# Kernel optimization log

Hardware: AMD Instinct MI355X
Metric: run time of the kernel (lower is better)

## Reference

```python
import jax, jax.numpy as jnp
import numpy as np

# Fixed problem sizes (equal-sized batch segments, matching setup_inputs)
B, N, M = 4, 4096, 16384          # clouds, coarse pts/cloud, fine pts/cloud
C_IN, C_SKIP, K = 256, 256, 3     # feature dims, knn k
CH = [C_IN + C_SKIP, 512, 256]    # MLP channels
EPS = 1e-16


def setup_inputs() -> dict:
    key = jax.random.key(0)
    ks = jax.random.split(key, 6)
    x = jax.random.normal(ks[0], (B * N, C_IN), jnp.float32)
    pos = jax.random.uniform(ks[1], (B * N, 3), jnp.float32)
    batch = jnp.repeat(jnp.arange(B, dtype=jnp.int64), N)
    x_skip = jax.random.normal(ks[2], (B * M, C_SKIP), jnp.float32)
    pos_skip = jax.random.uniform(ks[3], (B * M, 3), jnp.float32)
    batch_skip = jnp.repeat(jnp.arange(B, dtype=jnp.int64), M)
    W1 = jax.random.normal(ks[4], (CH[0], CH[1]), jnp.float32) / np.sqrt(CH[0]).astype(np.float32)
    b1 = jnp.zeros((CH[1],), jnp.float32)
    W2 = jax.random.normal(ks[5], (CH[1], CH[2]), jnp.float32) / np.sqrt(CH[1]).astype(np.float32)
    b2 = jnp.zeros((CH[2],), jnp.float32)
    return dict(x=x, pos=pos, batch=batch, x_skip=x_skip, pos_skip=pos_skip,
                batch_skip=batch_skip, W1=W1, b1=b1, W2=W2, b2=b2)


def _knn_interpolate(x, pos, pos_skip):
    """torch_geometric.nn.knn_interpolate with equal-sized batch segments."""
    xb = x.reshape(B, N, C_IN)
    ps = pos.reshape(B, N, 3)
    qs = pos_skip.reshape(B, M, 3)
    # squared pairwise distances [B, M, N]
    d2 = (jnp.sum(qs * qs, -1)[:, :, None]
          - 2.0 * jnp.einsum('bmd,bnd->bmn', qs, ps)
          + jnp.sum(ps * ps, -1)[:, None, :])
    neg_d2, idx = jax.lax.top_k(-d2, K)                # k smallest distances, [B,M,K]
    w = 1.0 / jnp.clip(-neg_d2, EPS)                   # inverse squared distance weights
    feats = jax.vmap(lambda f, i: f[i])(xb, idx)       # gather: [B, M, K, C_IN]
    y = jnp.sum(w[..., None] * feats, axis=2) / jnp.sum(w, axis=2)[..., None]
    return y.reshape(B * M, C_IN)


def reference(x, pos, batch, x_skip, pos_skip, batch_skip, W1, b1, W2, b2):
    y = _knn_interpolate(x, pos, pos_skip)
    h = jnp.concatenate([y, x_skip], axis=1)           # [B*M, 512]
    h = jax.nn.relu(h @ W1 + b1)
    h = jax.nn.relu(h @ W2 + b2)
    return h, pos_skip, batch_skip
```

## Files before the change

kernel.cpp:

```cpp
#include <hip/hip_runtime.h>
#include <stdint.h>

#define NB 4
#define NPTS 4096
#define MPTS 16384
#define CIN 256
#define CH0 512
#define CH1 512
#define CH2 256
#define ROWS (NB * MPTS)
#define POS_OUT_OFF (ROWS * CH2)
#define BATCH_OUT_OFF (POS_OUT_OFF + ROWS * 3)
#define CELL_CAP 40
#define QCAP 96

using u16 = unsigned short;
using u32 = unsigned int;
using u64 = unsigned long long;

typedef __bf16 bf16x8 __attribute__((ext_vector_type(8)));
typedef float f32x4 __attribute__((ext_vector_type(4)));

__device__ __forceinline__ u16 f2bf(float f) {
  u32 u = __builtin_bit_cast(u32, f);
  u32 r = u + 0x7fffu + ((u >> 16) & 1u);
  return (u16)(r >> 16);
}

__device__ __forceinline__ u32 flipf(float f) {
  u32 u = __builtin_bit_cast(u32, f);
  return u ^ ((u32)((int)u >> 31) | 0x80000000u);
}
__device__ __forceinline__ float unflipf(u32 f) {
  u32 m = (~(u32)((int)f >> 31)) | 0x80000000u;
  return __builtin_bit_cast(float, f ^ m);
}

__device__ __forceinline__ void ins3(u64 v, u64& k0, u64& k1, u64& k2) {
  u64 a = k0 < v ? v : k0;
  k0 = k0 < v ? k0 : v;
  u64 bb = k1 < a ? a : k1;
  k1 = k1 < a ? k1 : a;
  k2 = k2 < bb ? k2 : bb;
}

__device__ __forceinline__ void merge3(u64 r0, u64 r1, u64 r2,
                                       u64& k0, u64& k1, u64& k2) {
  u64 t = k0 < r0 ? r0 : k0;
  k0 = k0 < r0 ? k0 : r0;
  u64 u = k1 < r1 ? k1 : r1;
  u64 mtu = t < u ? u : t;
  k1 = t < u ? t : u;
  u64 v = k2 < r2 ? k2 : r2;
  k2 = mtu < v ? mtu : v;
}

__device__ __forceinline__ u64 shfl_xor_u64_w8(u64 v, int mask) {
  u32 lo = (u32)v, hi = (u32)(v >> 32);
  lo = (u32)__shfl_xor((int)lo, mask, 8);
  hi = (u32)__shfl_xor((int)hi, mask, 8);
  return ((u64)hi << 32) | lo;
}

__global__ __launch_bounds__(256) void preptail_kernel(
    const float* __restrict__ W1, const float* __restrict__ W2,
    u16* __restrict__ W1s, u16* __restrict__ W2s,
    const float* __restrict__ pos_skip, const int* __restrict__ batch_skip,
    float* __restrict__ out) {
  const int bid = blockIdx.x;
  if (bid < 192) {
    const int t = bid * 256 + threadIdx.x;
    if (t < 32768) {
      const int l = t & 63, ni = (t >> 6) & 3, wd = (t >> 8) & 7, kt = t >> 11;
      const int fr = l & 15, g = l >> 4;
      const int n = wd * 64 + ni * 16 + fr;
      u16 o[8];
#pragma unroll
      for (int j = 0; j < 8; ++j)
        o[j] = f2bf(W1[(kt * 32 + g * 8 + j) * CH1 + n]);
      *(uint4*)(W1s + (size_t)t * 8) = *(const uint4*)o;
    } else {
      const int c = t - 32768;
      const int l = c & 63, ni = (c >> 6) & 1, wd = (c >> 7) & 7, kt = c >> 10;
      const int fr = l & 15, g = l >> 4;
      const int n = wd * 32 + ni * 16 + fr;
      u16 o[8];
#pragma unroll
      for (int j = 0; j < 8; ++j)
        o[j] = f2bf(W2[(kt * 32 + g * 8 + j) * CH2 + n]);
      *(uint4*)(W2s + (size_t)c * 8) = *(const uint4*)o;
    }
  } else {
    const int t = (bid - 192) * 256 + threadIdx.x;
    if (t < ROWS * 3) {
      out[POS_OUT_OFF + t] = pos_skip[t];
    } else {
      int u = t - ROWS * 3;
      out[BATCH_OUT_OFF + u] = (float)batch_skip[u];
    }
  }
}

__global__ __launch_bounds__(256) void bin_kernel(
    const float* __restrict__ pos, float4* __restrict__ pts4,
    u32* __restrict__ cellCnt, int* __restrict__ cellIdx,
    const float* __restrict__ pos_skip, u32* __restrict__ qCnt,
    int* __restrict__ qIdx) {
#pragma clang fp contract(off)
  if (blockIdx.x < 64) {
    const int i = blockIdx.x * 256 + threadIdx.x;
    const float x = pos[i * 3 + 0], y = pos[i * 3 + 1], z = pos[i * 3 + 2];
    pts4[i] = make_float4(x, y, z, (x * x + y * y) + z * z);
    const int b = i >> 12;
    int cx = (int)(x * 8.0f); cx = cx < 0 ? 0 : (cx > 7 ? 7 : cx);
    int cy = (int)(y * 8.0f); cy = cy < 0 ? 0 : (cy > 7 ? 7 : cy);
    int cz = (int)(z * 8.0f); cz = cz < 0 ? 0 : (cz > 7 ? 7 : cz);
    const int c = b * 512 + cz * 64 + cy * 8 + cx;
    const u32 slot = atomicAdd(&cellCnt[c], 1u);
    if (slot < CELL_CAP) cellIdx[c * CELL_CAP + slot] = i;
  } else {
    const int q = (blockIdx.x - 64) * 256 + threadIdx.x;
    const int b = q >> 14;
    const float qx = pos_skip[q * 3 + 0];
    const float qy = pos_skip[q * 3 + 1];
    const float qz = pos_skip[q * 3 + 2];
    int cx = (int)(qx * 8.0f); cx = cx < 0 ? 0 : (cx > 7 ? 7 : cx);
    int cy = (int)(qy * 8.0f); cy = cy < 0 ? 0 : (cy > 7 ? 7 : cy);
    int cz = (int)(qz * 8.0f); cz = cz < 0 ? 0 : (cz > 7 ? 7 : cz);
    const int c = b * 512 + cz * 64 + cy * 8 + cx;
    const u32 slot = atomicAdd(&qCnt[c], 1u);
    if (slot < QCAP) qIdx[c * QCAP + slot] = q;
  }
}

__global__ __launch_bounds__(256) void knn_kernel(
    const float4* __restrict__ pts4, const u32* __restrict__ cellCnt,
    const int* __restrict__ cellIdx, const u32* __restrict__ qCnt,
    const int* __restrict__ qIdx, const float* __restrict__ pos_skip,
    int* __restrict__ idx_out, float* __restrict__ w_out,
    int* __restrict__ qPerm) {
#pragma clang fp contract(off)
  __shared__ float4 scand[27 * CELL_CAP];
  __shared__ int    scgi[27 * CELL_CAP];
  __shared__ u32    scnt[27];
  __shared__ int    sbase[27];
  __shared__ u32    nCand;
  __shared__ u32    ssc[256];
  const int tid = threadIdx.x;

  if (blockIdx.x >= 2048) {
    const int b = blockIdx.x - 2048;
    u32 c0 = qCnt[b * 512 + 2 * tid];     c0 = c0 > QCAP ? QCAP : c0;
    u32 c1 = qCnt[b * 512 + 2 * tid + 1]; c1 = c1 > QCAP ? QCAP : c1;
    const u32 ps = c0 + c1;
    u32 run = ps;
    ssc[tid] = run;
    for (int off = 1; off < 256; off <<= 1) {
      __syncthreads();
      u32 t = (tid >= off) ? ssc[tid - off] : 0u;
      __syncthreads();
      run += t;
      ssc[tid] = run;
    }
    const u32 excl = run - ps;
    const int base = b * MPTS + (int)excl;
    const int s0 = (b * 512 + 2 * tid) * QCAP;
    const int s1 = (b * 512 + 2 * tid + 1) * QCAP;
    for (u32 j = 0; j < c0; ++j) qPerm[base + j] = qIdx[s0 + j];
    for (u32 j = 0; j < c1; ++j) qPerm[base + c0 + j] = qIdx[s1 + j];
    return;
  }

  const int b = blockIdx.x >> 9;
  const int cell = blockIdx.x & 511;
  const int cz = cell >> 6, cy = (cell >> 3) & 7, cx = cell & 7;
  const int x0 = cx > 0 ? cx - 1 : 0, x1 = cx < 7 ? cx + 1 : 7;
  const int y0 = cy > 0 ? cy - 1 : 0, y1 = cy < 7 ? cy + 1 : 7;
  const int z0 = cz > 0 ? cz - 1 : 0, z1 = cz < 7 ? cz + 1 : 7;
  const int nx = x1 - x0 + 1, ny = y1 - y0 + 1, nz = z1 - z0 + 1;
  const int ncells = nx * ny * nz;
  if (tid == 0) nCand = 0;
  if (tid < ncells) {
    const int lz = tid / (nx * ny);
    const int rem = tid - lz * nx * ny;
    const int ly = rem / nx;
    const int lx = rem - ly * nx;
    const int cg = b * 512 + (z0 + lz) * 64 + (y0 + ly) * 8 + (x0 + lx);
    u32 cnt = cellCnt[cg];
    scnt[tid] = cnt > CELL_CAP ? CELL_CAP : cnt;
    sbase[tid] = cg * CELL_CAP;
  }
  __syncthreads();
  const int slots = ncells * CELL_CAP;
  for (int s = tid; s < slots; s += 256) {
    const int ci = s / CELL_CAP;
    const int sl = s - ci * CELL_CAP;
    if ((u32)sl < scnt[ci]) {
      const int gi = cellIdx[sbase[ci] + sl];
      const float4 p = pts4[gi];
      const u32 d = atomicAdd(&nCand, 1u);
      scand[d] = p;
      scgi[d] = gi;
    }
  }
  __syncthreads();
  const int nC = (int)nCand;
  u32 nq = qCnt[b * 512 + cell];
  if (nq > QCAP) nq = QCAP;
  const int qbase = (b * 512 + cell) * QCAP;
  const int g = tid >> 3;
  const int sub = tid & 7;

  for (int r0q = 0; r0q < (int)nq; r0q += 32) {
    const int qslot = r0q + g;
    if (qslot < (int)nq) {
      const int q = qIdx[qbase + qslot];
      const float qx = pos_skip[q * 3 + 0];
      const float qy = pos_skip[q * 3 + 1];
      const float qz = pos_skip[q * 3 + 2];
      const float q2 = (qx * qx + qy * qy) + qz * qz;
      u64 k0 = ~0ull, k1 = ~0ull, k2 = ~0ull;
      for (int s = sub; s < nC; s += 8) {
        const float4 p = scand[s];
        const float dot = fmaf(qz, p.z, fmaf(qy, p.y, qx * p.x));
        const float tv = (q2 - 2.0f * dot) + p.w;
        const u64 key = ((u64)flipf(tv) << 32) | (u32)scgi[s];
        ins3(key, k0, k1, k2);
      }
#pragma unroll
      for (int mask = 1; mask < 8; mask <<= 1) {
        const u64 r0 = shfl_xor_u64_w8(k0, mask);
        const u64 r1 = shfl_xor_u64_w8(k1, mask);
        const u64 r2 = shfl_xor_u64_w8(k2, mask);
        merge3(r0, r1, r2, k0, k1, k2);
      }
      float m2tv = unflipf((u32)(k2 >> 32));
      if (!(m2tv <= 0.015625f - 1e-5f)) {
        k0 = k1 = k2 = ~0ull;
        const int ex0 = cx > 1 ? cx - 2 : 0, ex1 = cx < 6 ? cx + 2 : 7;
        const int ey0 = cy > 1 ? cy - 2 : 0, ey1 = cy < 6 ? cy + 2 : 7;
        const int ez0 = cz > 1 ? cz - 2 : 0, ez1 = cz < 6 ? cz + 2 : 7;
        for (int zz = ez0; zz <= ez1; ++zz)
          for (int yy = ey0; yy <= ey1; ++yy)
            for (int xx = ex0; xx <= ex1; ++xx) {
              const int cg = b * 512 + zz * 64 + yy * 8 + xx;
              u32 cnt = cellCnt[cg];
              if (cnt > CELL_CAP) cnt = CELL_CAP;
              const int cb = cg * CELL_CAP;
              for (int s = sub; s < (int)cnt; s += 8) {
                const int gi = cellIdx[cb + s];
                const float4 p = pts4[gi];
                const float dot = fmaf(qz, p.z, fmaf(qy, p.y, qx * p.x));
                const float tv = (q2 - 2.0f * dot) + p.w;
                ins3(((u64)flipf(tv) << 32) | (u32)gi, k0, k1, k2);
              }
            }
#pragma unroll
        for (int mask = 1; mask < 8; mask <<= 1) {
          const u64 r0 = shfl_xor_u64_w8(k0, mask);
          const u64 r1 = shfl_xor_u64_w8(k1, mask);
          const u64 r2 = shfl_xor_u64_w8(k2, mask);
          merge3(r0, r1, r2, k0, k1, k2);
        }
        m2tv = unflipf((u32)(k2 >> 32));
        if (!(m2tv <= 0.0625f - 1e-5f)) {
          k0 = k1 = k2 = ~0ull;
          const int base = b * NPTS;
          for (int i = sub; i < NPTS; i += 8) {
            const int gi = base + i;
            const float4 p = pts4[gi];
            const float dot = fmaf(qz, p.z, fmaf(qy, p.y, qx * p.x));
            const float tv = (q2 - 2.0f * dot) + p.w;
            ins3(((u64)flipf(tv) << 32) | (u32)gi, k0, k1, k2);
          }
#pragma unroll
          for (int mask = 1; mask < 8; mask <<= 1) {
            const u64 r0 = shfl_xor_u64_w8(k0, mask);
            const u64 r1 = shfl_xor_u64_w8(k1, mask);
            const u64 r2 = shfl_xor_u64_w8(k2, mask);
            merge3(r0, r1, r2, k0, k1, k2);
          }
        }
      }
      if (sub == 0) {
        const float t0 = unflipf((u32)(k0 >> 32));
        const float t1 = unflipf((u32)(k1 >> 32));
        const float t2 = unflipf((u32)(k2 >> 32));
        const float w0 = 1.0f / fmaxf(t0, 1e-16f);
        const float w1 = 1.0f / fmaxf(t1, 1e-16f);
        const float w2 = 1.0f / fmaxf(t2, 1e-16f);
        const float wsum = (w0 + w1) + w2;
        const float inv = 1.0f / wsum;
        idx_out[q * 3 + 0] = (int)(u32)k0;
        idx_out[q * 3 + 1] = (int)(u32)k1;
        idx_out[q * 3 + 2] = (int)(u32)k2;
        w_out[q * 3 + 0] = w0 * inv;
        w_out[q * 3 + 1] = w1 * inv;
        w_out[q * 3 + 2] = w2 * inv;
      }
    }
  }
}

__global__ __launch_bounds__(512, 2) void fused_mlp_kernel(
    const float* __restrict__ x, const int* __restrict__ idx,
    const float* __restrict__ w, const float* __restrict__ x_skip,
    const u16* __restrict__ W1s, const float* __restrict__ b1,
    const u16* __restrict__ W2s, const float* __restrict__ b2,
    const int* __restrict__ qPerm, float* __restrict__ out) {
  __shared__ __align__(16) u16 Abuf[128 * 512];
  __shared__ int sPerm[128];
  const int tid = threadIdx.x;
  const int m0 = blockIdx.x * 128;

  if (tid < 128) sPerm[tid] = qPerm[m0 + tid];

#pragma unroll
  for (int p = 0; p < 2; ++p) {
    const int row = p * 64 + (tid >> 3);
    const int sub = tid & 7;
    const int gr = qPerm[m0 + row];
    u16* rowp = Abuf + row * 512;
    const int rx = row & 7;
    if (sub < 4) {
      const int i0 = idx[gr * 3 + 0], i1 = idx[gr * 3 + 1], i2 = idx[gr * 3 + 2];
      const float w0 = w[gr * 3 + 0], w1 = w[gr * 3 + 1], w2 = w[gr * 3 + 2];
      const float4* p0 = (const float4*)(x + (size_t)i0 * CIN + sub * 64);
      const float4* p1 = (const float4*)(x + (size_t)i1 * CIN + sub * 64);
      const float4* p2 = (const float4*)(x + (size_t)i2 * CIN + sub * 64);
#pragma unroll
      for (int c = 0; c < 8; ++c) {
        const float4 a0 = p0[c * 2], a1 = p1[c * 2], a2 = p2[c * 2];
        const float4 d0 = p0[c * 2 + 1], d1 = p1[c * 2 + 1], d2 = p2[c * 2 + 1];
        u16 o[8];
        o[0] = f2bf(fmaf(w0, a0.x, fmaf(w1, a1.x, w2 * a2.x)));
        o[1] = f2bf(fmaf(w0, a0.y, fmaf(w1, a1.y, w2 * a2.y)));
        o[2] = f2bf(fmaf(w0, a0.z, fmaf(w1, a1.z, w2 * a2.z)));
        o[3] = f2bf(fmaf(w0, a0.w, fmaf(w1, a1.w, w2 * a2.w)));
        o[4] = f2bf(fmaf(w0, d0.x, fmaf(w1, d1.x, w2 * d2.x)));
        o[5] = f2bf(fmaf(w0, d0.y, fmaf(w1, d1.y, w2 * d2.y)));
        o[6] = f2bf(fmaf(w0, d0.z, fmaf(w1, d1.z, w2 * d2.z)));
        o[7] = f2bf(fmaf(w0, d0.w, fmaf(w1, d1.w, w2 * d2.w)));
        const int pp = ((c & 3) << 3) | (((2 * sub + (c >> 2)) ^ rx) & 7);
        *(uint4*)(rowp + pp * 8) = *(const uint4*)o;
      }
    } else {
      const int ss = sub - 4;
      const float4* ps = (const float4*)(x_skip + (size_t)gr * CIN + ss * 64);
#pragma unroll
      for (int c = 0; c < 8; ++c) {
        const float4 a = ps[c * 2], d = ps[c * 2 + 1];
        u16 o[8];
        o[0] = f2bf(a.x); o[1] = f2bf(a.y); o[2] = f2bf(a.z); o[3] = f2bf(a.w);
        o[4] = f2bf(d.x); o[5] = f2bf(d.y); o[6] = f2bf(d.z); o[7] = f2bf(d.w);
        const int pp = 32 | ((c & 3) << 3) | (((2 * ss + (c >> 2)) ^ rx) & 7);
        *(uint4*)(rowp + pp * 8) = *(const uint4*)o;
      }
    }
  }
  __syncthreads();

  const int wid = tid >> 6;
  const int lane = tid & 63;
  const int fr = lane & 15;
  const int g = lane >> 4;
  const int frx = fr & 7;

  f32x4 acc[8][4];
#pragma unroll
  for (int mi = 0; mi < 8; mi++)
#pragma unroll
    for (int ni = 0; ni < 4; ni++) acc[mi][ni] = (f32x4){0.f, 0.f, 0.f, 0.f};

  {
    const u16* B1 = W1s + wid * 2048 + lane * 8;
    bf16x8 bf[2][4];
#pragma unroll
    for (int ni = 0; ni < 4; ni++)
      bf[0][ni] = *(const bf16x8*)(B1 + ni * 512);
    for (int kt = 0; kt < 16; ++kt) {
      const int cur = kt & 1;
      if (kt < 15) {
        const u16* nb = B1 + (kt + 1) * 16384;
#pragma unroll
        for (int ni = 0; ni < 4; ni++)
          bf[cur ^ 1][ni] = *(const bf16x8*)(nb + ni * 512);
      }
#pragma unroll
      for (int mi = 0; mi < 8; mi++) {
        const bf16x8 af = *(const bf16x8*)&Abuf[(mi * 16 + fr) * 512 +
            ((((kt >> 3) << 5) | (g << 3) | ((kt & 7) ^ frx)) * 8)];
#pragma unroll
        for (int ni = 0; ni < 4; ni++)
          acc[mi][ni] = __builtin_amdgcn_mfma_f32_16x16x32_bf16(
              af, bf[cur][ni], acc[mi][ni], 0, 0, 0);
      }
    }
  }
  __syncthreads();

  {
    const int wn = wid * 64;
#pragma unroll
    for (int ni = 0; ni < 4; ni++) {
      const int n = wn + ni * 16 + fr;
      const float bb = b1[n];
      const int vg = n >> 3;
      const int nlow = n & 7;
      const int pb = (vg & 32) | ((vg & 3) << 3) | ((vg >> 2) & 7);
#pragma unroll
      for (int mi = 0; mi < 8; mi++) {
#pragma unroll
        for (int r = 0; r < 4; r++) {
          const int m = mi * 16 + g * 4 + r;
          const float v = fmaxf(acc[mi][ni][r] + bb, 0.f);
          Abuf[m * 512 + (pb ^ (m & 7)) * 8 + nlow] = f2bf(v);
        }
      }
    }
  }
  __syncthreads();

  f32x4 acc2[8][2];
#pragma unroll
  for (int mi = 0; mi < 8; mi++)
#pragma unroll
    for (int ni = 0; ni < 2; ni++) acc2[mi][ni] = (f32x4){0.f, 0.f, 0.f, 0.f};

  {
    const u16* B2 = W2s + wid * 1024 + lane * 8;
    bf16x8 bf[2][2];
#pragma unroll
    for (int ni = 0; ni < 2; ni++)
      bf[0][ni] = *(const bf16x8*)(B2 + ni * 512);
    for (int kt = 0; kt < 16; ++kt) {
      const int cur = kt & 1;
      if (kt < 15) {
        const u16* nb = B2 + (kt + 1) * 8192;
#pragma unroll
        for (int ni = 0; ni < 2; ni++)
          bf[cur ^ 1][ni] = *(const bf16x8*)(nb + ni * 512);
      }
#pragma unroll
      for (int mi = 0; mi < 8; mi++) {
        const bf16x8 af = *(const bf16x8*)&Abuf[(mi * 16 + fr) * 512 +
            ((((kt >> 3) << 5) | (g << 3) | ((kt & 7) ^ frx)) * 8)];
#pragma unroll
        for (int ni = 0; ni < 2; ni++)
          acc2[mi][ni] = __builtin_amdgcn_mfma_f32_16x16x32_bf16(
              af, bf[cur][ni], acc2[mi][ni], 0, 0, 0);
      }
    }
  }

#pragma unroll
  for (int ni = 0; ni < 2; ni++) {
    const int col = wid * 32 + ni * 16 + fr;
    const float bb = b2[col];
#pragma unroll
    for (int mi = 0; mi < 8; mi++) {
#pragma unroll
      for (int r = 0; r < 4; r++) {
        const int rowg = sPerm[mi * 16 + g * 4 + r];
        out[(size_t)rowg * CH2 + col] = fmaxf(acc2[mi][ni][r] + bb, 0.f);
      }
    }
  }
}

extern "C" void kernel_launch(void* const* d_in, const int* in_sizes, int n_in,
                              void* d_out, int out_size, void* d_ws, size_t ws_size,
                              hipStream_t stream) {
  const float* x        = (const float*)d_in[0];
  const float* pos      = (const float*)d_in[1];
  const float* x_skip   = (const float*)d_in[3];
  const float* pos_skip = (const float*)d_in[4];
  const int*   batch_sk = (const int*)d_in[5];
  const float* W1       = (const float*)d_in[6];
  const float* b1       = (const float*)d_in[7];
  const float* W2       = (const float*)d_in[8];
  const float* b2       = (const float*)d_in[9];
  float* out = (float*)d_out;

  char* ws = (char*)d_ws;
  u16*    W1s     = (u16*)(ws);
  u16*    W2s     = (u16*)(ws + 524288);
  int*    idxb    = (int*)(ws + 786432);
  float*  wb      = (float*)(ws + 1572864);
  float4* pts4    = (float4*)(ws + 2359296);
  u32*    cellCnt = (u32*)(ws + 2621440);
  u32*    qCnt    = (u32*)(ws + 2629632);
  int*    cellIdx = (int*)(ws + 2637824);
  int*    qIdx    = (int*)(ws + 2965504);
  int*    qPerm   = (int*)(ws + 3751936);

  hipMemsetAsync(cellCnt, 0, 16384, stream);
  preptail_kernel<<<dim3(1216), dim3(256), 0, stream>>>(
      W1, W2, W1s, W2s, pos_skip, batch_sk, out);
  bin_kernel<<<dim3(320), dim3(256), 0, stream>>>(
      pos, pts4, cellCnt, cellIdx, pos_skip, qCnt, qIdx);
  knn_kernel<<<dim3(2052), dim3(256), 0, stream>>>(pts4, cellCnt, cellIdx,
                                                   qCnt, qIdx, pos_skip,
                                                   idxb, wb, qPerm);
  fused_mlp_kernel<<<dim3(512), dim3(512), 0, stream>>>(
      x, idxb, wb, x_skip, W1s, b1, W2s, b2, qPerm, out);
}
```

Before: 263.7 us.

## Deduplicate kNN neighbor gathers via shared-memory hash and halve MLP row tile

The fused MLP kernel now processes 64 rows per block instead of 128, launching twice as many blocks. For each 32-row half it builds a small shared-memory hash table of unique neighbor indices, loads each unique coarse feature row once as bf16 into LDS, then interpolates from LDS. It also prefetches all A fragments before the MFMA loop. The aim is to cut redundant global gathers for spatially sorted queries and to improve occupancy and load balance. The cost is more barriers and atomics, halved weight reuse per block, and interpolating from bf16-rounded inputs, which adds a little extra rounding.

```diff
diff --git a/kernel.cpp b/kernel.cpp
--- a/kernel.cpp
+++ b/kernel.cpp
@@ -25,6 +25,10 @@
   u32 u = __builtin_bit_cast(u32, f);
   u32 r = u + 0x7fffu + ((u >> 16) & 1u);
   return (u16)(r >> 16);
+}
+
+__device__ __forceinline__ float bf2f(u16 h) {
+  return __builtin_bit_cast(float, (u32)h << 16);
 }
 
 __device__ __forceinline__ u32 flipf(float f) {
@@ -302,63 +306,111 @@
   }
 }
 
-__global__ __launch_bounds__(512, 2) void fused_mlp_kernel(
+__global__ __launch_bounds__(512) void fused_mlp_kernel(
     const float* __restrict__ x, const int* __restrict__ idx,
     const float* __restrict__ w, const float* __restrict__ x_skip,
     const u16* __restrict__ W1s, const float* __restrict__ b1,
     const u16* __restrict__ W2s, const float* __restrict__ b2,
     const int* __restrict__ qPerm, float* __restrict__ out) {
-  __shared__ __align__(16) u16 Abuf[128 * 512];
-  __shared__ int sPerm[128];
+  __shared__ __align__(16) u16 Abuf[64 * 512];
+  __shared__ __align__(16) u16 Xs[96 * 264];
+  __shared__ int   sPerm[64];
+  __shared__ float sWt[96];
+  __shared__ int   sSlot[96];
+  __shared__ int   hKey[128];
+  __shared__ int   hVal[128];
+  __shared__ int   uList[96];
+  __shared__ u32   uCnt;
   const int tid = threadIdx.x;
-  const int m0 = blockIdx.x * 128;
-
-  if (tid < 128) sPerm[tid] = qPerm[m0 + tid];
-
-#pragma unroll
+  const int m0 = blockIdx.x * 64;
+
+  if (tid < 64) sPerm[tid] = qPerm[m0 + tid];
+
   for (int p = 0; p < 2; ++p) {
-    const int row = p * 64 + (tid >> 3);
-    const int sub = tid & 7;
-    const int gr = qPerm[m0 + row];
-    u16* rowp = Abuf + row * 512;
-    const int rx = row & 7;
-    if (sub < 4) {
-      const int i0 = idx[gr * 3 + 0], i1 = idx[gr * 3 + 1], i2 = idx[gr * 3 + 2];
-      const float w0 = w[gr * 3 + 0], w1 = w[gr * 3 + 1], w2 = w[gr * 3 + 2];
-      const float4* p0 = (const float4*)(x + (size_t)i0 * CIN + sub * 64);
-      const float4* p1 = (const float4*)(x + (size_t)i1 * CIN + sub * 64);
-      const float4* p2 = (const float4*)(x + (size_t)i2 * CIN + sub * 64);
-#pragma unroll
-      for (int c = 0; c < 8; ++c) {
-        const float4 a0 = p0[c * 2], a1 = p1[c * 2], a2 = p2[c * 2];
-        const float4 d0 = p0[c * 2 + 1], d1 = p1[c * 2 + 1], d2 = p2[c * 2 + 1];
+    if (tid < 128) hKey[tid] = -1;
+    if (tid == 0) uCnt = 0;
+    __syncthreads();
+    int myH = 0;
+    if (tid < 96) {
+      const int r = tid / 3, k = tid - r * 3;
+      const int q = sPerm[p * 32 + r];
+      const int key = idx[q * 3 + k];
+      sWt[tid] = w[q * 3 + k];
+      u32 h = (((u32)key * 2654435761u) >> 25) & 127u;
+      for (;;) {
+        const int prev = atomicCAS(&hKey[h], -1, key);
+        if (prev == -1) {
+          const int s = (int)atomicAdd(&uCnt, 1u);
+          hVal[h] = s;
+          uList[s] = key;
+          myH = (int)h;
+          break;
+        }
+        if (prev == key) { myH = (int)h; break; }
+        h = (h + 1) & 127u;
+      }
+    }
+    __syncthreads();
+    const int U = (int)uCnt;
+    if (tid < 96) sSlot[tid] = hVal[myH];
+    if (tid < 256) {
+      for (int j = tid; j < U * 64; j += 256) {
+        const int u = j >> 6, seg = j & 63;
+        const float4 v = ((const float4*)x)[(size_t)uList[u] * 64 + seg];
+        u16 o[4] = {f2bf(v.x), f2bf(v.y), f2bf(v.z), f2bf(v.w)};
+        *(uint2*)&Xs[u * 264 + seg * 4] = *(const uint2*)o;
+      }
+    } else {
+      const int t2 = tid - 256;
+      for (int j = t2; j < 32 * 64; j += 256) {
+        const int r = j >> 6, seg = j & 63;
+        const int row = p * 32 + r;
+        const float4 v = ((const float4*)x_skip)[(size_t)sPerm[row] * 64 + seg];
+        u16 o[4] = {f2bf(v.x), f2bf(v.y), f2bf(v.z), f2bf(v.w)};
+        const int s5 = seg >> 1;
+        const int c = s5 & 3, ss = s5 >> 2;
+        const int pp = 32 | (c << 3) | ((ss ^ (row & 7)) & 7);
+        *(uint2*)&Abuf[row * 512 + pp * 8 + (seg & 1) * 4] = *(const uint2*)o;
+      }
+    }
+    __syncthreads();
+    if (tid < 256) {
+      const int r = tid >> 3, sub = tid & 7;
+      const int row = p * 32 + r;
+      const int e = r * 3;
+      const int s0 = sSlot[e], s1 = sSlot[e + 1], s2 = sSlot[e + 2];
+      const float w0 = sWt[e], w1 = sWt[e + 1], w2 = sWt[e + 2];
+      const u16* x0 = &Xs[s0 * 264 + sub * 32];
+      const u16* x1 = &Xs[s1 * 264 + sub * 32];
+      const u16* x2 = &Xs[s2 * 264 + sub * 32];
+      const int rx = row & 7;
+      u16* rowp = Abuf + row * 512;
+#pragma unroll
+      for (int c = 0; c < 4; ++c) {
+        const uint4 v0 = *(const uint4*)(x0 + c * 8);
+        const uint4 v1 = *(const uint4*)(x1 + c * 8);
+        const uint4 v2 = *(const uint4*)(x2 + c * 8);
+        const u32 a0[4] = {v0.x, v0.y, v0.z, v0.w};
+        const u32 a1[4] = {v1.x, v1.y, v1.z, v1.w};
+        const u32 a2[4] = {v2.x, v2.y, v2.z, v2.w};
         u16 o[8];
-        o[0] = f2bf(fmaf(w0, a0.x, fmaf(w1, a1.x, w2 * a2.x)));
-        o[1] = f2bf(fmaf(w0, a0.y, fmaf(w1, a1.y, w2 * a2.y)));
-        o[2] = f2bf(fmaf(w0, a0.z, fmaf(w1, a1.z, w2 * a2.z)));
-        o[3] = f2bf(fmaf(w0, a0.w, fmaf(w1, a1.w, w2 * a2.w)));
-        o[4] = f2bf(fmaf(w0, d0.x, fmaf(w1, d1.x, w2 * d2.x)));
-        o[5] = f2bf(fmaf(w0, d0.y, fmaf(w1, d1.y, w2 * d2.y)));
-        o[6] = f2bf(fmaf(w0, d0.z, fmaf(w1, d1.z, w2 * d2.z)));
-        o[7] = f2bf(fmaf(w0, d0.w, fmaf(w1, d1.w, w2 * d2.w)));
-        const int pp = ((c & 3) << 3) | (((2 * sub + (c >> 2)) ^ rx) & 7);
+#pragma unroll
+        for (int jj = 0; jj < 4; ++jj) {
+          const float lo = fmaf(w0, __builtin_bit_cast(float, a0[jj] << 16),
+                          fmaf(w1, __builtin_bit_cast(float, a1[jj] << 16),
+                          w2 * __builtin_bit_cast(float, a2[jj] << 16)));
+          const float hi = fmaf(w0, __builtin_bit_cast(float, a0[jj] & 0xffff0000u),
+                          fmaf(w1, __builtin_bit_cast(float, a1[jj] & 0xffff0000u),
+                          w2 * __builtin_bit_cast(float, a2[jj] & 0xffff0000u)));
+          o[jj * 2]     = f2bf(lo);
+          o[jj * 2 + 1] = f2bf(hi);
+        }
+        const int pp = (c << 3) | ((sub ^ rx) & 7);
         *(uint4*)(rowp + pp * 8) = *(const uint4*)o;
       }
-    } else {
-      const int ss = sub - 4;
-      const float4* ps = (const float4*)(x_skip + (size_t)gr * CIN + ss * 64);
-#pragma unroll
-      for (int c = 0; c < 8; ++c) {
-        const float4 a = ps[c * 2], d = ps[c * 2 + 1];
-        u16 o[8];
-        o[0] = f2bf(a.x); o[1] = f2bf(a.y); o[2] = f2bf(a.z); o[3] = f2bf(a.w);
-        o[4] = f2bf(d.x); o[5] = f2bf(d.y); o[6] = f2bf(d.z); o[7] = f2bf(d.w);
-        const int pp = 32 | ((c & 3) << 3) | (((2 * ss + (c >> 2)) ^ rx) & 7);
-        *(uint4*)(rowp + pp * 8) = *(const uint4*)o;
-      }
-    }
-  }
-  __syncthreads();
+    }
+    __syncthreads();
+  }
 
   const int wid = tid >> 6;
   const int lane = tid & 63;
@@ -366,9 +418,9 @@
   const int g = lane >> 4;
   const int frx = fr & 7;
 
-  f32x4 acc[8][4];
-#pragma unroll
-  for (int mi = 0; mi < 8; mi++)
+  f32x4 acc[4][4];
+#pragma unroll
+  for (int mi = 0; mi < 4; mi++)
 #pragma unroll
     for (int ni = 0; ni < 4; ni++) acc[mi][ni] = (f32x4){0.f, 0.f, 0.f, 0.f};
 
@@ -386,15 +438,17 @@
         for (int ni = 0; ni < 4; ni++)
           bf[cur ^ 1][ni] = *(const bf16x8*)(nb + ni * 512);
       }
-#pragma unroll
-      for (int mi = 0; mi < 8; mi++) {
-        const bf16x8 af = *(const bf16x8*)&Abuf[(mi * 16 + fr) * 512 +
+      bf16x8 af[4];
+#pragma unroll
+      for (int mi = 0; mi < 4; mi++)
+        af[mi] = *(const bf16x8*)&Abuf[(mi * 16 + fr) * 512 +
             ((((kt >> 3) << 5) | (g << 3) | ((kt & 7) ^ frx)) * 8)];
+#pragma unroll
+      for (int mi = 0; mi < 4; mi++)
 #pragma unroll
         for (int ni = 0; ni < 4; ni++)
           acc[mi][ni] = __builtin_amdgcn_mfma_f32_16x16x32_bf16(
-              af, bf[cur][ni], acc[mi][ni], 0, 0, 0);
-      }
+              af[mi], bf[cur][ni], acc[mi][ni], 0, 0, 0);
     }
   }
   __syncthreads();
@@ -409,7 +463,7 @@
       const int nlow = n & 7;
       const int pb = (vg & 32) | ((vg & 3) << 3) | ((vg >> 2) & 7);
 #pragma unroll
-      for (int mi = 0; mi < 8; mi++) {
+      for (int mi = 0; mi < 4; mi++) {
 #pragma unroll
         for (int r = 0; r < 4; r++) {
           const int m = mi * 16 + g * 4 + r;
@@ -421,9 +475,9 @@
   }
   __syncthreads();
 
-  f32x4 acc2[8][2];
-#pragma unroll
-  for (int mi = 0; mi < 8; mi++)
+  f32x4 acc2[4][2];
+#pragma unroll
+  for (int mi = 0; mi < 4; mi++)
 #pragma unroll
     for (int ni = 0; ni < 2; ni++) acc2[mi][ni] = (f32x4){0.f, 0.f, 0.f, 0.f};
 
@@ -441,15 +495,17 @@
         for (int ni = 0; ni < 2; ni++)
           bf[cur ^ 1][ni] = *(const bf16x8*)(nb + ni * 512);
       }
-#pragma unroll
-      for (int mi = 0; mi < 8; mi++) {
-        const bf16x8 af = *(const bf16x8*)&Abuf[(mi * 16 + fr) * 512 +
+      bf16x8 af[4];
+#pragma unroll
+      for (int mi = 0; mi < 4; mi++)
+        af[mi] = *(const bf16x8*)&Abuf[(mi * 16 + fr) * 512 +
             ((((kt >> 3) << 5) | (g << 3) | ((kt & 7) ^ frx)) * 8)];
+#pragma unroll
+      for (int mi = 0; mi < 4; mi++)
 #pragma unroll
         for (int ni = 0; ni < 2; ni++)
           acc2[mi][ni] = __builtin_amdgcn_mfma_f32_16x16x32_bf16(
-              af, bf[cur][ni], acc2[mi][ni], 0, 0, 0);
-      }
+              af[mi], bf[cur][ni], acc2[mi][ni], 0, 0, 0);
     }
   }
 
@@ -458,7 +514,7 @@
     const int col = wid * 32 + ni * 16 + fr;
     const float bb = b2[col];
 #pragma unroll
-    for (int mi = 0; mi < 8; mi++) {
+    for (int mi = 0; mi < 4; mi++) {
 #pragma unroll
       for (int r = 0; r < 4; r++) {
         const int rowg = sPerm[mi * 16 + g * 4 + r];
@@ -502,6 +558,6 @@
   knn_kernel<<<dim3(2052), dim3(256), 0, stream>>>(pts4, cellCnt, cellIdx,
                                                    qCnt, qIdx, pos_skip,
                                                    idxb, wb, qPerm);
-  fused_mlp_kernel<<<dim3(512), dim3(512), 0, stream>>>(
+  fused_mlp_kernel<<<dim3(1024), dim3(512), 0, stream>>>(
       x, idxb, wb, x_skip, W1s, b1, W2s, b2, qPerm, out);
 }
```

Measured after the change: 266.0 us. About the same (+0.8%).
